# Kernel optimization log

Hardware: AMD Instinct MI355X
Metric: run time of the kernel (lower is better)

The kernel has to match this reference:

```python
import jax, jax.numpy as jnp
import numpy as np
from jax.scipy.special import logsumexp

B, M, N = 512, 256, 256
ITERS = 20


def setup_inputs() -> dict:
    key = jax.random.key(0)
    k1, = jax.random.split(key, 1)
    scores = jax.random.normal(k1, (B, M, N), dtype=jnp.float32)
    alpha = jnp.ones((1,), dtype=jnp.float32)  # dustbin_weights parameter
    return {"scores": scores, "alpha": alpha, "iters": ITERS}


def reference(scores, alpha, iters):
    b, m, n = scores.shape
    a = alpha.reshape(())
    # Augment with dustbin row/column -> couplings [b, m+1, n+1]
    bins0 = jnp.broadcast_to(a, (b, m, 1))
    bins1 = jnp.broadcast_to(a, (b, 1, n))
    corner = jnp.broadcast_to(a, (b, 1, 1))
    couplings = jnp.concatenate(
        [jnp.concatenate([scores, bins0], axis=2),
         jnp.concatenate([bins1, corner], axis=2)], axis=1)

    ms = jnp.asarray(m, scores.dtype)
    ns = jnp.asarray(n, scores.dtype)
    norm = -jnp.log(ms + ns)  # scalar
    log_mu = jnp.concatenate([jnp.full((m,), norm, scores.dtype),
                              (jnp.log(ns) + norm)[None]])  # [m+1]
    log_nu = jnp.concatenate([jnp.full((n,), norm, scores.dtype),
                              (jnp.log(ms) + norm)[None]])  # [n+1]
    log_mu = jnp.broadcast_to(log_mu[None], (b, m + 1))
    log_nu = jnp.broadcast_to(log_nu[None], (b, n + 1))

    u0 = jnp.zeros_like(log_mu)
    v0 = jnp.zeros_like(log_nu)

    def body(carry, _):
        u, v = carry
        u = log_mu - logsumexp(couplings + v[:, None, :], axis=2)
        v = log_nu - logsumexp(couplings + u[:, :, None], axis=1)
        return (u, v), None

    (u, v), _ = jax.lax.scan(body, (u0, v0), None, length=iters)
    Z = couplings + u[:, :, None] + v[:, None, :]
    return Z - norm
```

## Files before the change

### kernel.cpp

```cpp
#include <hip/hip_runtime.h>


typedef _Float16 half8 __attribute__((ext_vector_type(8)));
typedef float floatx4 __attribute__((ext_vector_type(4)));

constexpr float L2E = 1.4426950408889634f;
constexpr float LN2 = 0.6931471805599453f;

__device__ __forceinline__ float flog2(float x) { return __builtin_amdgcn_logf(x); }
__device__ __forceinline__ float fexp2(float x) { return __builtin_amdgcn_exp2f(x); }

__device__ __forceinline__ float rcp_nr(float d) {
    float r = __builtin_amdgcn_rcpf(d);
    return r * fmaf(-d, r, 2.0f);
}

template <int CTRL>
__device__ __forceinline__ float dpp_add(float x) {
    int y = __builtin_amdgcn_update_dpp(0, __builtin_bit_cast(int, x), CTRL, 0xF, 0xF, true);
    return x + __builtin_bit_cast(float, y);
}
__device__ __forceinline__ float reduce16(float x) {
    x = dpp_add<0xB1>(x);
    x = dpp_add<0x4E>(x);
    x = dpp_add<0x124>(x);
    x = dpp_add<0x128>(x);
    return x;
}
__device__ __forceinline__ float xor16_add(float x) {
    int y = __builtin_amdgcn_ds_swizzle(__builtin_bit_cast(int, x), 0x401F);
    return x + __builtin_bit_cast(float, y);
}

__global__ __launch_bounds__(1024)
__attribute__((amdgpu_waves_per_eu(4, 4)))
void sinkhorn_kernel(const float* __restrict__ scores,
                     const float* __restrict__ alpha_p,
                     const int* __restrict__ iters_p,
                     float* __restrict__ out)
{
    const int bat = blockIdx.x;
    const int t   = threadIdx.x;
    const int a   = t >> 5;
    const int bb  = t & 31;
    const int w   = t >> 6;
    const int l   = t & 63;
    const int g   = (t >> 4) & 3;
    const int l15 = t & 15;

    const float alpha2 = alpha_p[0] * L2E;
    const float A  = fexp2(alpha2);
    const float Cs = fexp2(8.0f - alpha2);
    const int iters = iters_p[0];

    __shared__ __align__(16) unsigned short esT[65536];
    __shared__ __align__(16) unsigned short EUa[272];
    __shared__ __align__(16) unsigned short EVa[272];
    __shared__ __align__(16) float wsU[16];
    __shared__ __align__(16) float wsV[16];

    {
        const float* sp = scores + ((size_t)bat << 16) + ((size_t)a << 11) + (bb << 2);
        half8 cp[8];
        #pragma unroll
        for (int r = 0; r < 8; ++r) {
            const float4 x0 = *reinterpret_cast<const float4*>(sp + (r << 8));
            const float4 x1 = *reinterpret_cast<const float4*>(sp + (r << 8) + 128);
            cp[0][r] = (_Float16)fexp2(x0.x * L2E);
            cp[1][r] = (_Float16)fexp2(x0.y * L2E);
            cp[2][r] = (_Float16)fexp2(x0.z * L2E);
            cp[3][r] = (_Float16)fexp2(x0.w * L2E);
            cp[4][r] = (_Float16)fexp2(x1.x * L2E);
            cp[5][r] = (_Float16)fexp2(x1.y * L2E);
            cp[6][r] = (_Float16)fexp2(x1.z * L2E);
            cp[7][r] = (_Float16)fexp2(x1.w * L2E);
        }
        #pragma unroll
        for (int ci = 0; ci < 8; ++ci) {
            const int col = (ci < 4) ? ((bb << 2) + ci) : (128 + (bb << 2) + ci - 4);
            const int idx = (col << 8) + (((a << 3)) ^ ((col & 7) << 3));
            *reinterpret_cast<half8*>(&esT[idx]) = cp[ci];
        }
    }
    if (t < 256) EVa[t] = 0x3C00;
    if (t < 16)  wsV[t] = 16.0f;
    __syncthreads();

    half8 esA[8];
    {
        const int m16 = (w << 4) + l15;
        #pragma unroll
        for (int s = 0; s < 8; ++s) {
            #pragma unroll
            for (int j = 0; j < 8; ++j) {
                const int col = (s << 5) + (g << 3) + j;
                const unsigned short v =
                    esT[(col << 8) + (m16 ^ ((col & 7) << 3))];
                esA[s][j] = __builtin_bit_cast(_Float16, v);
            }
            asm volatile("" : "+v"(esA[s]));
        }
    }

    float evd = 1.0f, eud_s = 1.0f;

    for (int it = 0; it < iters; ++it) {
        float sv = evd;
        {
            const floatx4* wv = reinterpret_cast<const floatx4*>(wsV);
            floatx4 s0 = wv[0], s1 = wv[1], s2 = wv[2], s3 = wv[3];
            floatx4 ss = (s0 + s1) + (s2 + s3);
            sv += (ss[0] + ss[1]) + (ss[2] + ss[3]);
        }
        eud_s = Cs * rcp_nr(sv);
        const float tdu = A * eud_s;
        const float tdv = A * evd;

        floatx4 acc = {0.f, 0.f, 0.f, 0.f};
        const half8* evp = reinterpret_cast<const half8*>(EVa) + g;
        #pragma unroll
        for (int s = 0; s < 8; ++s)
            acc = __builtin_amdgcn_mfma_f32_16x16x32_f16(esA[s], evp[s << 2], acc, 0, 0, 0);

        const float E0 = rcp_nr(acc[0] + tdv);
        const float E1 = rcp_nr(acc[1] + tdv);
        const float E2 = rcp_nr(acc[2] + tdv);
        const float E3 = rcp_nr(acc[3] + tdv);
        if (l15 < 4) {
            const float lo = (l15 & 1) ? E1 : E0;
            const float hi = (l15 & 1) ? E3 : E2;
            const float val = (l15 & 2) ? hi : lo;
            EUa[(w << 4) + (g << 2) + l15] =
                __builtin_bit_cast(unsigned short, (_Float16)val);
        }
        float sU = (E0 + E1) + (E2 + E3);
        sU = xor16_add(sU);
        sU += __shfl_xor(sU, 32, 64);
        if (l == 0) wsU[w] = sU;
        __syncthreads();

        float su = eud_s;
        {
            const floatx4* wu = reinterpret_cast<const floatx4*>(wsU);
            floatx4 s0 = wu[0], s1 = wu[1], s2 = wu[2], s3 = wu[3];
            floatx4 ss = (s0 + s1) + (s2 + s3);
            su += (ss[0] + ss[1]) + (ss[2] + ss[3]);
        }
        evd = Cs * rcp_nr(su);

        floatx4 acc2 = {0.f, 0.f, 0.f, 0.f};
        const int cbase = ((w << 4) + l15) << 8;
        const int swq = (l15 & 7) << 3;
        const half8* eup = reinterpret_cast<const half8*>(EUa) + g;
        #pragma unroll
        for (int s = 0; s < 8; ++s) {
            const half8 bq = *reinterpret_cast<const half8*>(
                &esT[cbase + (((s << 5) + (g << 3)) ^ swq)]);
            acc2 = __builtin_amdgcn_mfma_f32_16x16x32_f16(eup[s << 2], bq, acc2, 0, 0, 0);
        }
        const float EVv = rcp_nr(acc2[0] + tdu);
        if (l < 16) EVa[(w << 4) + l] =
            __builtin_bit_cast(unsigned short, (_Float16)EVv);
        float sV = reduce16(EVv);
        if (l == 0) wsV[w] = sV;
        __syncthreads();
    }

    const float Ud = flog2(eud_s);
    const float Vd = flog2(evd);
    float Up[8], Vp[8];
    int cols[8];
    #pragma unroll
    for (int r = 0; r < 8; ++r)
        Up[r] = flog2((float)__builtin_bit_cast(_Float16, EUa[(a << 3) + r]));
    #pragma unroll
    for (int ci = 0; ci < 8; ++ci) {
        cols[ci] = (ci < 4) ? ((bb << 2) + ci) : (128 + (bb << 2) + ci - 4);
        Vp[ci] = flog2((float)__builtin_bit_cast(_Float16, EVa[cols[ci]]));
    }
    const size_t ob = (size_t)bat * 66049;
    #pragma unroll
    for (int ci = 0; ci < 8; ++ci) {
        const int col = cols[ci];
        const half8 esc = *reinterpret_cast<const half8*>(
            &esT[(col << 8) + ((a << 3) ^ ((col & 7) << 3))]);
        #pragma unroll
        for (int r = 0; r < 8; ++r) {
            out[ob + (size_t)((a << 3) + r) * 257 + col] =
                (flog2((float)esc[r]) + Up[r] + Vp[ci]) * LN2;
        }
    }
    if (bb == 0) {
        #pragma unroll
        for (int r = 0; r < 8; ++r)
            out[ob + (size_t)((a << 3) + r) * 257 + 256] =
                (alpha2 + Up[r] + Vd) * LN2;
    }
    if (t < 257) {
        const float vp = (t < 256)
            ? flog2((float)__builtin_bit_cast(_Float16, EVa[t])) : Vd;
        out[ob + 65792 + t] = (alpha2 + Ud + vp) * LN2;
    }
}

extern "C" void kernel_launch(void* const* d_in, const int* in_sizes, int n_in,
                              void* d_out, int out_size, void* d_ws, size_t ws_size,
                              hipStream_t stream)
{
    const float* scores = (const float*)d_in[0];
    const float* alpha  = (const float*)d_in[1];
    const int*   iters  = (const int*)d_in[2];
    float* out = (float*)d_out;
    const int B = in_sizes[0] >> 16;
    hipLaunchKernelGGL(sinkhorn_kernel, dim3(B), dim3(1024), 0, stream,
                       scores, alpha, iters, out);
}
```

Measured before the change: 112.9 us.

## Cache column fragments in registers, split MFMA chains, compute sums from fragments

Holds the transposed coupling fragments (esB) in registers for the whole iteration loop, so the per-iteration LDS reads from esT go away. Each MFMA accumulation is split into four independent chains that are summed at the end, which shortens the dependency chain. The dustbin normalization sums are now computed redundantly in every wave from the fp16 u/v fragments already loaded, which removes the wsU/wsV shared reductions. The epilogue writes from register fragments row by row. The costs are extra VGPR pressure, fp16 rounding inside the sums, and a different store pattern.

```diff
diff --git a/kernel.cpp b/kernel.cpp
--- a/kernel.cpp
+++ b/kernel.cpp
@@ -15,21 +15,21 @@
     return r * fmaf(-d, r, 2.0f);
 }
 
-template <int CTRL>
-__device__ __forceinline__ float dpp_add(float x) {
-    int y = __builtin_amdgcn_update_dpp(0, __builtin_bit_cast(int, x), CTRL, 0xF, 0xF, true);
-    return x + __builtin_bit_cast(float, y);
-}
-__device__ __forceinline__ float reduce16(float x) {
-    x = dpp_add<0xB1>(x);
-    x = dpp_add<0x4E>(x);
-    x = dpp_add<0x124>(x);
-    x = dpp_add<0x128>(x);
-    return x;
-}
 __device__ __forceinline__ float xor16_add(float x) {
     int y = __builtin_amdgcn_ds_swizzle(__builtin_bit_cast(int, x), 0x401F);
     return x + __builtin_bit_cast(float, y);
+}
+__device__ __forceinline__ float gsum(float x) {
+    x = xor16_add(x);
+    x += __shfl_xor(x, 32, 64);
+    return x;
+}
+__device__ __forceinline__ float fragsum(const half8* f) {
+    half8 a = (f[0] + f[1]) + (f[2] + f[3]);
+    half8 b = (f[4] + f[5]) + (f[6] + f[7]);
+    half8 c = a + b;
+    return (((float)c[0] + (float)c[1]) + ((float)c[2] + (float)c[3]))
+         + (((float)c[4] + (float)c[5]) + ((float)c[6] + (float)c[7]));
 }
 
 __global__ __launch_bounds__(1024)
@@ -56,8 +56,6 @@
     __shared__ __align__(16) unsigned short esT[65536];
     __shared__ __align__(16) unsigned short EUa[272];
     __shared__ __align__(16) unsigned short EVa[272];
-    __shared__ __align__(16) float wsU[16];
-    __shared__ __align__(16) float wsV[16];
 
     {
         const float* sp = scores + ((size_t)bat << 16) + ((size_t)a << 11) + (bb << 2);
@@ -83,7 +81,6 @@
         }
     }
     if (t < 256) EVa[t] = 0x3C00;
-    if (t < 16)  wsV[t] = 16.0f;
     __syncthreads();
 
     half8 esA[8];
@@ -101,101 +98,96 @@
             asm volatile("" : "+v"(esA[s]));
         }
     }
+    half8 esB[8];
+    {
+        const int cbase = ((w << 4) + l15) << 8;
+        const int swq = (l15 & 7) << 3;
+        #pragma unroll
+        for (int s = 0; s < 8; ++s) {
+            esB[s] = *reinterpret_cast<const half8*>(
+                &esT[cbase + (((s << 5) + (g << 3)) ^ swq)]);
+            asm volatile("" : "+v"(esB[s]));
+        }
+    }
 
     float evd = 1.0f, eud_s = 1.0f;
+    float tdv = A;
+
+    const half8* evp = reinterpret_cast<const half8*>(EVa) + g;
+    const half8* eup = reinterpret_cast<const half8*>(EUa) + g;
 
     for (int it = 0; it < iters; ++it) {
-        float sv = evd;
-        {
-            const floatx4* wv = reinterpret_cast<const floatx4*>(wsV);
-            floatx4 s0 = wv[0], s1 = wv[1], s2 = wv[2], s3 = wv[3];
-            floatx4 ss = (s0 + s1) + (s2 + s3);
-            sv += (ss[0] + ss[1]) + (ss[2] + ss[3]);
-        }
-        eud_s = Cs * rcp_nr(sv);
+        half8 evf[8];
+        #pragma unroll
+        for (int s = 0; s < 8; ++s) evf[s] = evp[s << 2];
+
+        floatx4 ac[4];
+        #pragma unroll
+        for (int k = 0; k < 4; ++k) ac[k] = (floatx4){0.f, 0.f, 0.f, 0.f};
+        #pragma unroll
+        for (int s = 0; s < 8; ++s)
+            ac[s & 3] = __builtin_amdgcn_mfma_f32_16x16x32_f16(esA[s], evf[s], ac[s & 3], 0, 0, 0);
+        const floatx4 acc = (ac[0] + ac[1]) + (ac[2] + ac[3]);
+
+        const float sv = gsum(fragsum(evf));
+        eud_s = Cs * rcp_nr(sv + evd);
         const float tdu = A * eud_s;
-        const float tdv = A * evd;
-
-        floatx4 acc = {0.f, 0.f, 0.f, 0.f};
-        const half8* evp = reinterpret_cast<const half8*>(EVa) + g;
-        #pragma unroll
-        for (int s = 0; s < 8; ++s)
-            acc = __builtin_amdgcn_mfma_f32_16x16x32_f16(esA[s], evp[s << 2], acc, 0, 0, 0);
 
         const float E0 = rcp_nr(acc[0] + tdv);
         const float E1 = rcp_nr(acc[1] + tdv);
         const float E2 = rcp_nr(acc[2] + tdv);
         const float E3 = rcp_nr(acc[3] + tdv);
         if (l15 < 4) {
-            const float lo = (l15 & 1) ? E1 : E0;
-            const float hi = (l15 & 1) ? E3 : E2;
+            const float lo  = (l15 & 1) ? E1 : E0;
+            const float hi  = (l15 & 1) ? E3 : E2;
             const float val = (l15 & 2) ? hi : lo;
             EUa[(w << 4) + (g << 2) + l15] =
                 __builtin_bit_cast(unsigned short, (_Float16)val);
         }
-        float sU = (E0 + E1) + (E2 + E3);
-        sU = xor16_add(sU);
-        sU += __shfl_xor(sU, 32, 64);
-        if (l == 0) wsU[w] = sU;
         __syncthreads();
 
-        float su = eud_s;
-        {
-            const floatx4* wu = reinterpret_cast<const floatx4*>(wsU);
-            floatx4 s0 = wu[0], s1 = wu[1], s2 = wu[2], s3 = wu[3];
-            floatx4 ss = (s0 + s1) + (s2 + s3);
-            su += (ss[0] + ss[1]) + (ss[2] + ss[3]);
-        }
-        evd = Cs * rcp_nr(su);
-
-        floatx4 acc2 = {0.f, 0.f, 0.f, 0.f};
-        const int cbase = ((w << 4) + l15) << 8;
-        const int swq = (l15 & 7) << 3;
-        const half8* eup = reinterpret_cast<const half8*>(EUa) + g;
-        #pragma unroll
-        for (int s = 0; s < 8; ++s) {
-            const half8 bq = *reinterpret_cast<const half8*>(
-                &esT[cbase + (((s << 5) + (g << 3)) ^ swq)]);
-            acc2 = __builtin_amdgcn_mfma_f32_16x16x32_f16(eup[s << 2], bq, acc2, 0, 0, 0);
-        }
+        half8 euf[8];
+        #pragma unroll
+        for (int s = 0; s < 8; ++s) euf[s] = eup[s << 2];
+
+        floatx4 qc[4];
+        #pragma unroll
+        for (int k = 0; k < 4; ++k) qc[k] = (floatx4){0.f, 0.f, 0.f, 0.f};
+        #pragma unroll
+        for (int s = 0; s < 8; ++s)
+            qc[s & 3] = __builtin_amdgcn_mfma_f32_16x16x32_f16(euf[s], esB[s], qc[s & 3], 0, 0, 0);
+        const floatx4 acc2 = (qc[0] + qc[1]) + (qc[2] + qc[3]);
+
+        const float su = gsum(fragsum(euf));
+        evd = Cs * rcp_nr(su + eud_s);
+        tdv = A * evd;
+
         const float EVv = rcp_nr(acc2[0] + tdu);
         if (l < 16) EVa[(w << 4) + l] =
             __builtin_bit_cast(unsigned short, (_Float16)EVv);
-        float sV = reduce16(EVv);
-        if (l == 0) wsV[w] = sV;
         __syncthreads();
     }
+
+    half8 evf[8];
+    #pragma unroll
+    for (int s = 0; s < 8; ++s) evf[s] = evp[s << 2];
 
     const float Ud = flog2(eud_s);
     const float Vd = flog2(evd);
-    float Up[8], Vp[8];
-    int cols[8];
+    const float Up_l = flog2((float)__builtin_bit_cast(_Float16, EUa[(w << 4) + l15]));
+    const int row = (w << 4) + l15;
+    const size_t ob = (size_t)bat * 66049;
+    float* rp = out + ob + (size_t)row * 257;
+
     #pragma unroll
-    for (int r = 0; r < 8; ++r)
-        Up[r] = flog2((float)__builtin_bit_cast(_Float16, EUa[(a << 3) + r]));
-    #pragma unroll
-    for (int ci = 0; ci < 8; ++ci) {
-        cols[ci] = (ci < 4) ? ((bb << 2) + ci) : (128 + (bb << 2) + ci - 4);
-        Vp[ci] = flog2((float)__builtin_bit_cast(_Float16, EVa[cols[ci]]));
-    }
-    const size_t ob = (size_t)bat * 66049;
-    #pragma unroll
-    for (int ci = 0; ci < 8; ++ci) {
-        const int col = cols[ci];
-        const half8 esc = *reinterpret_cast<const half8*>(
-            &esT[(col << 8) + ((a << 3) ^ ((col & 7) << 3))]);
-        #pragma unroll
-        for (int r = 0; r < 8; ++r) {
-            out[ob + (size_t)((a << 3) + r) * 257 + col] =
-                (flog2((float)esc[r]) + Up[r] + Vp[ci]) * LN2;
-        }
-    }
-    if (bb == 0) {
-        #pragma unroll
-        for (int r = 0; r < 8; ++r)
-            out[ob + (size_t)((a << 3) + r) * 257 + 256] =
-                (alpha2 + Up[r] + Vd) * LN2;
-    }
+    for (int s = 0; s < 8; ++s) {
+        const int c0 = (s << 5) + (g << 3);
+        #pragma unroll
+        for (int j = 0; j < 8; ++j) {
+            rp[c0 + j] = (flog2((float)esA[s][j]) + Up_l + flog2((float)evf[s][j])) * LN2;
+        }
+    }
+    if (l < 16) rp[256] = (alpha2 + Up_l + Vd) * LN2;
     if (t < 257) {
         const float vp = (t < 256)
             ? flog2((float)__builtin_bit_cast(_Float16, EVa[t])) : Vd;
```

After: 126.1 us. +11.8%, slower.
